# Kernel optimization log

Hardware: AMD Instinct MI355X
Metric: run time of the kernel (lower is better)

Reference implementation:

```python
import jax, jax.numpy as jnp
import numpy as np

NITER = 20
TOL = 1e-10


def setup_inputs() -> dict:
    key = jax.random.key(0)
    n = 8192
    kA, kR, kX = jax.random.split(key, 3)
    # SPD, well-conditioned system matrix: M = A A^T / n + I
    A = jax.random.normal(kA, (n, n), dtype=jnp.float32) * np.float32(1.0 / np.sqrt(n))
    M = A @ A.T + jnp.eye(n, dtype=jnp.float32)
    RHS = jax.random.normal(kR, (n,), dtype=jnp.float32)
    X = jax.random.normal(kX, (n,), dtype=jnp.float32)  # only its shape is used (zeros_like)
    return {"X": X, "M": M, "RHS": RHS}


def reference(X, M, RHS):
    # Faithful port of the TF while_loop CG: max NITER iterations,
    # early-stop condition rTr > 1e-10 emulated by freezing the state
    # (where-select) once converged, keeping fixed shapes under jit.
    X0 = jnp.zeros_like(X)
    r0 = RHS - M @ X0
    p0 = r0
    rTr0 = jnp.sum(r0 * r0)

    def body(carry, _):
        rTr, Xc, r, p = carry
        Ap = M @ p                      # [n] matvec, dominant cost
        rtr = jnp.sum(r * r)            # recomputed in loop body, as in TF source
        alpha = rtr / jnp.sum(p * Ap)
        Xn = Xc + alpha * p
        rn = r - alpha * Ap
        beta = jnp.sum(rn * rn) / rtr
        pn = rn + beta * p
        rTrn = jnp.sum(rn * rn)
        active = rTr > TOL              # while_loop cond on rTr from previous iter
        sel = lambda new, old: jnp.where(active, new, old)
        return (sel(rTrn, rTr), sel(Xn, Xc), sel(rn, r), sel(pn, p)), None

    (_, Xf, _, _), _ = jax.lax.scan(body, (rTr0, X0, r0, p0), None, length=NITER)
    return Xf
```

## Files before the change

### kernel.cpp

```cpp
#include <hip/hip_runtime.h>

#define N 8192
#define NITER 20
#define TOLF 1e-10f

typedef float floatx4 __attribute__((ext_vector_type(4)));
typedef unsigned int uintx4 __attribute__((ext_vector_type(4)));

__device__ __forceinline__ unsigned short f2bf_rne(float f) {
  unsigned int u = __float_as_uint(f);
  unsigned int r = u + 0x7fffu + ((u >> 16) & 1u);
  return (unsigned short)(r >> 16);
}
__device__ __forceinline__ unsigned int pk_bf2(float lo, float hi) {
  return (unsigned int)f2bf_rne(lo) | ((unsigned int)f2bf_rne(hi) << 16);
}
__device__ __forceinline__ float bflo(unsigned int u) { return __uint_as_float(u << 16); }
__device__ __forceinline__ float bfhi(unsigned int u) { return __uint_as_float(u & 0xffff0000u); }

__global__ __launch_bounds__(256) void init_kernel(
    const float* __restrict__ RHS, float* __restrict__ x, float* __restrict__ r,
    float* __restrict__ p, float* __restrict__ rt0) {
  int i = blockIdx.x * 256 + threadIdx.x;
  float v = RHS[i];
  x[i] = 0.0f;
  r[i] = v;
  p[i] = v;
  float val = v * v;
  for (int off = 32; off > 0; off >>= 1) val += __shfl_down(val, off, 64);
  __shared__ float bs[4];
  int wave = threadIdx.x >> 6, lane = threadIdx.x & 63;
  if (lane == 0) bs[wave] = val;
  __syncthreads();
  if (threadIdx.x == 0) atomicAdd(rt0, bs[0] + bs[1] + bs[2] + bs[3]);
}

__device__ __forceinline__ void finish_iteration(
    float* __restrict__ p, float* __restrict__ x, float* __restrict__ r,
    float* __restrict__ Ap, const float* __restrict__ rt,
    float* __restrict__ pap, float* __restrict__ rt_next,
    int* __restrict__ counter, float acc0, float acc1, int row0) {
  int wave = threadIdx.x >> 6, lane = threadIdx.x & 63;
  for (int off = 32; off > 0; off >>= 1) {
    acc0 += __shfl_down(acc0, off, 64);
    acc1 += __shfl_down(acc1, off, 64);
  }
  __shared__ float bs[16];
  __shared__ int tick;
  if (lane == 0) {
    Ap[row0]     = acc0;
    Ap[row0 + 1] = acc1;
    bs[wave] = p[row0] * acc0 + p[row0 + 1] * acc1;
  }
  __syncthreads();
  if (threadIdx.x == 0) {
    float S = 0.0f;
#pragma unroll
    for (int w = 0; w < 16; ++w) S += bs[w];
    __hip_atomic_fetch_add(pap, S, __ATOMIC_RELAXED, __HIP_MEMORY_SCOPE_AGENT);
    tick = __hip_atomic_fetch_add(counter, 1, __ATOMIC_ACQ_REL, __HIP_MEMORY_SCOPE_AGENT);
  }
  __syncthreads();
  if (tick != (int)gridDim.x - 1) return;

  float rtv = *rt;
  bool act = rtv > TOLF;
  if (!act) {
    if (threadIdx.x == 0) *rt_next = rtv;
    return;
  }
  float papv = __hip_atomic_load(pap, __ATOMIC_RELAXED, __HIP_MEMORY_SCOPE_AGENT);
  float alpha = rtv / papv;
  float val = 0.0f;
#pragma unroll
  for (int j = threadIdx.x * 4; j < N; j += 4096) {
    floatx4 pv = *(const floatx4*)(p + j);
    floatx4 av = *(const floatx4*)(Ap + j);
    floatx4 xv = *(const floatx4*)(x + j);
    floatx4 rv = *(const floatx4*)(r + j);
    xv += alpha * pv;
    rv -= alpha * av;
    *(floatx4*)(x + j) = xv;
    *(floatx4*)(r + j) = rv;
    val += rv.x * rv.x + rv.y * rv.y + rv.z * rv.z + rv.w * rv.w;
  }
  for (int off = 32; off > 0; off >>= 1) val += __shfl_down(val, off, 64);
  __shared__ float rs[17];
  if (lane == 0) rs[wave] = val;
  __syncthreads();
  if (threadIdx.x == 0) {
    float S = 0.0f;
#pragma unroll
    for (int w = 0; w < 16; ++w) S += rs[w];
    rs[16] = S;
    *rt_next = S;
  }
  __syncthreads();
  float beta = rs[16] / rtv;
#pragma unroll
  for (int j = threadIdx.x * 4; j < N; j += 4096) {
    floatx4 rv = *(const floatx4*)(r + j);
    floatx4 pv = *(const floatx4*)(p + j);
    pv = rv + beta * pv;
    *(floatx4*)(p + j) = pv;
  }
}

__global__ __launch_bounds__(1024, 4) void cg_iter0_cast(
    const float* __restrict__ M, unsigned short* __restrict__ Mb,
    const float* __restrict__ RHS, float* __restrict__ p, float* __restrict__ Ap,
    float* __restrict__ x, float* __restrict__ r, const float* __restrict__ rt,
    float* __restrict__ pap, float* __restrict__ rt_next, int* __restrict__ counter) {
  int wave = threadIdx.x >> 6, lane = threadIdx.x & 63;
  int row0 = blockIdx.x * 32 + wave * 2;
  const float* M0 = M + (size_t)row0 * N;
  const float* M1 = M0 + N;
  unsigned short* B0 = Mb + (size_t)row0 * N;
  unsigned short* B1 = B0 + N;
  float acc0 = 0.0f, acc1 = 0.0f;
#pragma unroll 2
  for (int c = lane * 8; c < N; c += 512) {
    floatx4 a0 = *(const floatx4*)(M0 + c);
    floatx4 a1 = *(const floatx4*)(M0 + c + 4);
    floatx4 b0 = *(const floatx4*)(M1 + c);
    floatx4 b1 = *(const floatx4*)(M1 + c + 4);
    floatx4 pa = *(const floatx4*)(RHS + c);
    floatx4 pb = *(const floatx4*)(RHS + c + 4);
    acc0 += a0.x * pa.x + a0.y * pa.y + a0.z * pa.z + a0.w * pa.w
          + a1.x * pb.x + a1.y * pb.y + a1.z * pb.z + a1.w * pb.w;
    acc1 += b0.x * pa.x + b0.y * pa.y + b0.z * pa.z + b0.w * pa.w
          + b1.x * pb.x + b1.y * pb.y + b1.z * pb.z + b1.w * pb.w;
    uintx4 o0 = {pk_bf2(a0.x, a0.y), pk_bf2(a0.z, a0.w),
                 pk_bf2(a1.x, a1.y), pk_bf2(a1.z, a1.w)};
    uintx4 o1 = {pk_bf2(b0.x, b0.y), pk_bf2(b0.z, b0.w),
                 pk_bf2(b1.x, b1.y), pk_bf2(b1.z, b1.w)};
    *(uintx4*)(B0 + c) = o0;
    *(uintx4*)(B1 + c) = o1;
  }
  finish_iteration(p, x, r, Ap, rt, pap, rt_next, counter, acc0, acc1, row0);
}

__global__ __launch_bounds__(1024, 4) void cg_iter(
    const unsigned short* __restrict__ Mb, float* __restrict__ p,
    float* __restrict__ Ap, float* __restrict__ x, float* __restrict__ r,
    const float* __restrict__ rt, float* __restrict__ pap,
    float* __restrict__ rt_next, int* __restrict__ counter) {
  int wave = threadIdx.x >> 6, lane = threadIdx.x & 63;
  int row0 = blockIdx.x * 32 + wave * 2;
  const unsigned short* M0 = Mb + (size_t)row0 * N;
  const unsigned short* M1 = M0 + N;
  float acc0 = 0.0f, acc1 = 0.0f;
#pragma unroll 4
  for (int c = lane * 8; c < N; c += 512) {
    uintx4 m0 = *(const uintx4*)(M0 + c);
    uintx4 m1 = *(const uintx4*)(M1 + c);
    floatx4 pa = *(const floatx4*)(p + c);
    floatx4 pb = *(const floatx4*)(p + c + 4);
    acc0 += bflo(m0.x) * pa.x + bfhi(m0.x) * pa.y
          + bflo(m0.y) * pa.z + bfhi(m0.y) * pa.w
          + bflo(m0.z) * pb.x + bfhi(m0.z) * pb.y
          + bflo(m0.w) * pb.z + bfhi(m0.w) * pb.w;
    acc1 += bflo(m1.x) * pa.x + bfhi(m1.x) * pa.y
          + bflo(m1.y) * pa.z + bfhi(m1.y) * pa.w
          + bflo(m1.z) * pb.x + bfhi(m1.z) * pb.y
          + bflo(m1.w) * pb.z + bfhi(m1.w) * pb.w;
  }
  finish_iteration(p, x, r, Ap, rt, pap, rt_next, counter, acc0, acc1, row0);
}

extern "C" void kernel_launch(void* const* d_in, const int* in_sizes, int n_in,
                              void* d_out, int out_size, void* d_ws, size_t ws_size,
                              hipStream_t stream) {
  const float* M   = (const float*)d_in[1];
  const float* RHS = (const float*)d_in[2];
  float* x = (float*)d_out;

  char* ws = (char*)d_ws;
  unsigned short* Mb = (unsigned short*)ws;
  float* Ap = (float*)(ws + (size_t)N * N * 2);
  float* r  = Ap + N;
  float* p  = r + N;
  float* sc = p + N;
  float* RT  = sc;
  float* PAP = sc + 21;
  int*   CNT = (int*)(sc + 41);

  (void)hipMemsetAsync(sc, 0, 61 * sizeof(float), stream);

  init_kernel<<<N / 256, 256, 0, stream>>>(RHS, x, r, p, &RT[0]);
  cg_iter0_cast<<<N / 32, 1024, 0, stream>>>(M, Mb, RHS, p, Ap, x, r,
                                             &RT[0], &PAP[0], &RT[1], &CNT[0]);
  for (int k = 1; k < NITER; ++k) {
    cg_iter<<<N / 32, 1024, 0, stream>>>(Mb, p, Ap, x, r,
                                         &RT[k], &PAP[k], &RT[k + 1], &CNT[k]);
  }
}
```

Measured before the change: 1.015 ms.

## Fuse CG iterations into one persistent cooperative kernel with grid barriers

Result: slower. 2.313 ms (+127.8%).

```diff
diff --git a/kernel.cpp b/kernel.cpp
--- a/kernel.cpp
+++ b/kernel.cpp
@@ -3,6 +3,7 @@
 #define N 8192
 #define NITER 20
 #define TOLF 1e-10f
+#define NBLK 256
 
 typedef float floatx4 __attribute__((ext_vector_type(4)));
 typedef unsigned int uintx4 __attribute__((ext_vector_type(4)));
@@ -18,154 +19,157 @@
 __device__ __forceinline__ float bflo(unsigned int u) { return __uint_as_float(u << 16); }
 __device__ __forceinline__ float bfhi(unsigned int u) { return __uint_as_float(u & 0xffff0000u); }
 
-__global__ __launch_bounds__(256) void init_kernel(
-    const float* __restrict__ RHS, float* __restrict__ x, float* __restrict__ r,
-    float* __restrict__ p, float* __restrict__ rt0) {
-  int i = blockIdx.x * 256 + threadIdx.x;
-  float v = RHS[i];
-  x[i] = 0.0f;
-  r[i] = v;
-  p[i] = v;
-  float val = v * v;
-  for (int off = 32; off > 0; off >>= 1) val += __shfl_down(val, off, 64);
-  __shared__ float bs[4];
-  int wave = threadIdx.x >> 6, lane = threadIdx.x & 63;
-  if (lane == 0) bs[wave] = val;
+__device__ __forceinline__ void grid_sync(int* cnt, int* gen) {
   __syncthreads();
-  if (threadIdx.x == 0) atomicAdd(rt0, bs[0] + bs[1] + bs[2] + bs[3]);
+  if (threadIdx.x == 0) {
+    int g = __hip_atomic_load(gen, __ATOMIC_RELAXED, __HIP_MEMORY_SCOPE_AGENT);
+    int t = __hip_atomic_fetch_add(cnt, 1, __ATOMIC_ACQ_REL, __HIP_MEMORY_SCOPE_AGENT);
+    if (t == NBLK - 1) {
+      __hip_atomic_store(cnt, 0, __ATOMIC_RELAXED, __HIP_MEMORY_SCOPE_AGENT);
+      __hip_atomic_fetch_add(gen, 1, __ATOMIC_ACQ_REL, __HIP_MEMORY_SCOPE_AGENT);
+    } else {
+      while (__hip_atomic_load(gen, __ATOMIC_ACQUIRE, __HIP_MEMORY_SCOPE_AGENT) == g)
+        __builtin_amdgcn_s_sleep(1);
+    }
+  }
+  __syncthreads();
 }
 
-__device__ __forceinline__ void finish_iteration(
-    float* __restrict__ p, float* __restrict__ x, float* __restrict__ r,
-    float* __restrict__ Ap, const float* __restrict__ rt,
-    float* __restrict__ pap, float* __restrict__ rt_next,
-    int* __restrict__ counter, float acc0, float acc1, int row0) {
+__device__ __forceinline__ float sum_part(const float* __restrict__ part, float* lred) {
+  float v = (threadIdx.x < NBLK) ? part[threadIdx.x] : 0.0f;
+  for (int off = 32; off > 0; off >>= 1) v += __shfl_down(v, off, 64);
   int wave = threadIdx.x >> 6, lane = threadIdx.x & 63;
-  for (int off = 32; off > 0; off >>= 1) {
-    acc0 += __shfl_down(acc0, off, 64);
-    acc1 += __shfl_down(acc1, off, 64);
-  }
-  __shared__ float bs[16];
-  __shared__ int tick;
-  if (lane == 0) {
-    Ap[row0]     = acc0;
-    Ap[row0 + 1] = acc1;
-    bs[wave] = p[row0] * acc0 + p[row0 + 1] * acc1;
-  }
+  if (lane == 0) lred[wave] = v;
   __syncthreads();
-  if (threadIdx.x == 0) {
-    float S = 0.0f;
-#pragma unroll
-    for (int w = 0; w < 16; ++w) S += bs[w];
-    __hip_atomic_fetch_add(pap, S, __ATOMIC_RELAXED, __HIP_MEMORY_SCOPE_AGENT);
-    tick = __hip_atomic_fetch_add(counter, 1, __ATOMIC_ACQ_REL, __HIP_MEMORY_SCOPE_AGENT);
-  }
+  float S = lred[0] + lred[1] + lred[2] + lred[3];
   __syncthreads();
-  if (tick != (int)gridDim.x - 1) return;
-
-  float rtv = *rt;
-  bool act = rtv > TOLF;
-  if (!act) {
-    if (threadIdx.x == 0) *rt_next = rtv;
-    return;
-  }
-  float papv = __hip_atomic_load(pap, __ATOMIC_RELAXED, __HIP_MEMORY_SCOPE_AGENT);
-  float alpha = rtv / papv;
-  float val = 0.0f;
-#pragma unroll
-  for (int j = threadIdx.x * 4; j < N; j += 4096) {
-    floatx4 pv = *(const floatx4*)(p + j);
-    floatx4 av = *(const floatx4*)(Ap + j);
-    floatx4 xv = *(const floatx4*)(x + j);
-    floatx4 rv = *(const floatx4*)(r + j);
-    xv += alpha * pv;
-    rv -= alpha * av;
-    *(floatx4*)(x + j) = xv;
-    *(floatx4*)(r + j) = rv;
-    val += rv.x * rv.x + rv.y * rv.y + rv.z * rv.z + rv.w * rv.w;
-  }
-  for (int off = 32; off > 0; off >>= 1) val += __shfl_down(val, off, 64);
-  __shared__ float rs[17];
-  if (lane == 0) rs[wave] = val;
-  __syncthreads();
-  if (threadIdx.x == 0) {
-    float S = 0.0f;
-#pragma unroll
-    for (int w = 0; w < 16; ++w) S += rs[w];
-    rs[16] = S;
-    *rt_next = S;
-  }
-  __syncthreads();
-  float beta = rs[16] / rtv;
-#pragma unroll
-  for (int j = threadIdx.x * 4; j < N; j += 4096) {
-    floatx4 rv = *(const floatx4*)(r + j);
-    floatx4 pv = *(const floatx4*)(p + j);
-    pv = rv + beta * pv;
-    *(floatx4*)(p + j) = pv;
-  }
+  return S;
 }
 
-__global__ __launch_bounds__(1024, 4) void cg_iter0_cast(
+__global__ __launch_bounds__(1024, 4) void cg_persistent(
     const float* __restrict__ M, unsigned short* __restrict__ Mb,
-    const float* __restrict__ RHS, float* __restrict__ p, float* __restrict__ Ap,
-    float* __restrict__ x, float* __restrict__ r, const float* __restrict__ rt,
-    float* __restrict__ pap, float* __restrict__ rt_next, int* __restrict__ counter) {
-  int wave = threadIdx.x >> 6, lane = threadIdx.x & 63;
-  int row0 = blockIdx.x * 32 + wave * 2;
-  const float* M0 = M + (size_t)row0 * N;
-  const float* M1 = M0 + N;
-  unsigned short* B0 = Mb + (size_t)row0 * N;
-  unsigned short* B1 = B0 + N;
-  float acc0 = 0.0f, acc1 = 0.0f;
+    const float* __restrict__ RHS, float* __restrict__ x,
+    float* __restrict__ Ap, float* __restrict__ r, float* __restrict__ p,
+    float* __restrict__ partA, float* __restrict__ partB,
+    int* __restrict__ cnt, int* __restrict__ gen) {
+  int b = blockIdx.x;
+  int t = threadIdx.x;
+  int wave = t >> 6, lane = t & 63;
+  __shared__ float lred[16];
+  __shared__ float bs[16];
+
+  {
+    float val = 0.0f;
+    if (t < 32) {
+      int i = b * 32 + t;
+      float v = RHS[i];
+      x[i] = 0.0f;
+      r[i] = v;
+      p[i] = v;
+      val = v * v;
+    }
+    for (int off = 32; off > 0; off >>= 1) val += __shfl_down(val, off, 64);
+    if (t == 0) partB[b] = val;
+  }
+  grid_sync(cnt, gen);
+  float rt = sum_part(partB, lred);
+
+  int row0 = b * 32 + wave * 2;
+
+  for (int k = 0; k < NITER; ++k) {
+    bool act = rt > TOLF;
+
+    if (act) {
+      float acc0 = 0.0f, acc1 = 0.0f;
+      if (k == 0) {
+        const float* M0 = M + (size_t)row0 * N;
+        const float* M1 = M0 + N;
+        unsigned short* B0 = Mb + (size_t)row0 * N;
+        unsigned short* B1 = B0 + N;
 #pragma unroll 2
-  for (int c = lane * 8; c < N; c += 512) {
-    floatx4 a0 = *(const floatx4*)(M0 + c);
-    floatx4 a1 = *(const floatx4*)(M0 + c + 4);
-    floatx4 b0 = *(const floatx4*)(M1 + c);
-    floatx4 b1 = *(const floatx4*)(M1 + c + 4);
-    floatx4 pa = *(const floatx4*)(RHS + c);
-    floatx4 pb = *(const floatx4*)(RHS + c + 4);
-    acc0 += a0.x * pa.x + a0.y * pa.y + a0.z * pa.z + a0.w * pa.w
-          + a1.x * pb.x + a1.y * pb.y + a1.z * pb.z + a1.w * pb.w;
-    acc1 += b0.x * pa.x + b0.y * pa.y + b0.z * pa.z + b0.w * pa.w
-          + b1.x * pb.x + b1.y * pb.y + b1.z * pb.z + b1.w * pb.w;
-    uintx4 o0 = {pk_bf2(a0.x, a0.y), pk_bf2(a0.z, a0.w),
-                 pk_bf2(a1.x, a1.y), pk_bf2(a1.z, a1.w)};
-    uintx4 o1 = {pk_bf2(b0.x, b0.y), pk_bf2(b0.z, b0.w),
-                 pk_bf2(b1.x, b1.y), pk_bf2(b1.z, b1.w)};
-    *(uintx4*)(B0 + c) = o0;
-    *(uintx4*)(B1 + c) = o1;
+        for (int c = lane * 8; c < N; c += 512) {
+          floatx4 a0 = *(const floatx4*)(M0 + c);
+          floatx4 a1 = *(const floatx4*)(M0 + c + 4);
+          floatx4 b0 = *(const floatx4*)(M1 + c);
+          floatx4 b1 = *(const floatx4*)(M1 + c + 4);
+          floatx4 pa = *(const floatx4*)(p + c);
+          floatx4 pb = *(const floatx4*)(p + c + 4);
+          acc0 += a0.x * pa.x + a0.y * pa.y + a0.z * pa.z + a0.w * pa.w
+                + a1.x * pb.x + a1.y * pb.y + a1.z * pb.z + a1.w * pb.w;
+          acc1 += b0.x * pa.x + b0.y * pa.y + b0.z * pa.z + b0.w * pa.w
+                + b1.x * pb.x + b1.y * pb.y + b1.z * pb.z + b1.w * pb.w;
+          uintx4 o0 = {pk_bf2(a0.x, a0.y), pk_bf2(a0.z, a0.w),
+                       pk_bf2(a1.x, a1.y), pk_bf2(a1.z, a1.w)};
+          uintx4 o1 = {pk_bf2(b0.x, b0.y), pk_bf2(b0.z, b0.w),
+                       pk_bf2(b1.x, b1.y), pk_bf2(b1.z, b1.w)};
+          *(uintx4*)(B0 + c) = o0;
+          *(uintx4*)(B1 + c) = o1;
+        }
+      } else {
+        const unsigned short* M0 = Mb + (size_t)row0 * N;
+        const unsigned short* M1 = M0 + N;
+#pragma unroll 4
+        for (int c = lane * 8; c < N; c += 512) {
+          uintx4 m0 = *(const uintx4*)(M0 + c);
+          uintx4 m1 = *(const uintx4*)(M1 + c);
+          floatx4 pa = *(const floatx4*)(p + c);
+          floatx4 pb = *(const floatx4*)(p + c + 4);
+          acc0 += bflo(m0.x) * pa.x + bfhi(m0.x) * pa.y
+                + bflo(m0.y) * pa.z + bfhi(m0.y) * pa.w
+                + bflo(m0.z) * pb.x + bfhi(m0.z) * pb.y
+                + bflo(m0.w) * pb.z + bfhi(m0.w) * pb.w;
+          acc1 += bflo(m1.x) * pa.x + bfhi(m1.x) * pa.y
+                + bflo(m1.y) * pa.z + bfhi(m1.y) * pa.w
+                + bflo(m1.z) * pb.x + bfhi(m1.z) * pb.y
+                + bflo(m1.w) * pb.z + bfhi(m1.w) * pb.w;
+        }
+      }
+      for (int off = 32; off > 0; off >>= 1) {
+        acc0 += __shfl_down(acc0, off, 64);
+        acc1 += __shfl_down(acc1, off, 64);
+      }
+      if (lane == 0) {
+        Ap[row0] = acc0;
+        Ap[row0 + 1] = acc1;
+        bs[wave] = p[row0] * acc0 + p[row0 + 1] * acc1;
+      }
+      __syncthreads();
+      if (t == 0) {
+        float S = 0.0f;
+#pragma unroll
+        for (int w = 0; w < 16; ++w) S += bs[w];
+        partA[b] = S;
+      }
+    }
+    grid_sync(cnt, gen);
+
+    if (act) {
+      float pap = sum_part(partA, lred);
+      float alpha = rt / pap;
+      float val = 0.0f;
+      if (t < 32) {
+        int i = b * 32 + t;
+        float rv = r[i] - alpha * Ap[i];
+        x[i] += alpha * p[i];
+        r[i] = rv;
+        val = rv * rv;
+      }
+      for (int off = 32; off > 0; off >>= 1) val += __shfl_down(val, off, 64);
+      if (t == 0) partB[b] = val;
+    }
+    grid_sync(cnt, gen);
+
+    if (act) {
+      float rnv = sum_part(partB, lred);
+      float beta = rnv / rt;
+      if (t < 32) {
+        int i = b * 32 + t;
+        p[i] = r[i] + beta * p[i];
+      }
+      rt = rnv;
+    }
+    grid_sync(cnt, gen);
   }
-  finish_iteration(p, x, r, Ap, rt, pap, rt_next, counter, acc0, acc1, row0);
-}
-
-__global__ __launch_bounds__(1024, 4) void cg_iter(
-    const unsigned short* __restrict__ Mb, float* __restrict__ p,
-    float* __restrict__ Ap, float* __restrict__ x, float* __restrict__ r,
-    const float* __restrict__ rt, float* __restrict__ pap,
-    float* __restrict__ rt_next, int* __restrict__ counter) {
-  int wave = threadIdx.x >> 6, lane = threadIdx.x & 63;
-  int row0 = blockIdx.x * 32 + wave * 2;
-  const unsigned short* M0 = Mb + (size_t)row0 * N;
-  const unsigned short* M1 = M0 + N;
-  float acc0 = 0.0f, acc1 = 0.0f;
-#pragma unroll 4
-  for (int c = lane * 8; c < N; c += 512) {
-    uintx4 m0 = *(const uintx4*)(M0 + c);
-    uintx4 m1 = *(const uintx4*)(M1 + c);
-    floatx4 pa = *(const floatx4*)(p + c);
-    floatx4 pb = *(const floatx4*)(p + c + 4);
-    acc0 += bflo(m0.x) * pa.x + bfhi(m0.x) * pa.y
-          + bflo(m0.y) * pa.z + bfhi(m0.y) * pa.w
-          + bflo(m0.z) * pb.x + bfhi(m0.z) * pb.y
-          + bflo(m0.w) * pb.z + bfhi(m0.w) * pb.w;
-    acc1 += bflo(m1.x) * pa.x + bfhi(m1.x) * pa.y
-          + bflo(m1.y) * pa.z + bfhi(m1.y) * pa.w
-          + bflo(m1.z) * pb.x + bfhi(m1.z) * pb.y
-          + bflo(m1.w) * pb.z + bfhi(m1.w) * pb.w;
-  }
-  finish_iteration(p, x, r, Ap, rt, pap, rt_next, counter, acc0, acc1, row0);
 }
 
 extern "C" void kernel_launch(void* const* d_in, const int* in_sizes, int n_in,
@@ -180,18 +184,16 @@
   float* Ap = (float*)(ws + (size_t)N * N * 2);
   float* r  = Ap + N;
   float* p  = r + N;
-  float* sc = p + N;
-  float* RT  = sc;
-  float* PAP = sc + 21;
-  int*   CNT = (int*)(sc + 41);
+  float* partA = p + N;
+  float* partB = partA + NBLK;
+  int* cnt = (int*)(partB + NBLK);
+  int* gen = cnt + 1;
 
-  (void)hipMemsetAsync(sc, 0, 61 * sizeof(float), stream);
+  (void)hipMemsetAsync(cnt, 0, 2 * sizeof(int), stream);
 
-  init_kernel<<<N / 256, 256, 0, stream>>>(RHS, x, r, p, &RT[0]);
-  cg_iter0_cast<<<N / 32, 1024, 0, stream>>>(M, Mb, RHS, p, Ap, x, r,
-                                             &RT[0], &PAP[0], &RT[1], &CNT[0]);
-  for (int k = 1; k < NITER; ++k) {
-    cg_iter<<<N / 32, 1024, 0, stream>>>(Mb, p, Ap, x, r,
-                                         &RT[k], &PAP[k], &RT[k + 1], &CNT[k]);
-  }
+  void* args[] = {(void*)&M, (void*)&Mb, (void*)&RHS, (void*)&x, (void*)&Ap,
+                  (void*)&r, (void*)&p, (void*)&partA, (void*)&partB,
+                  (void*)&cnt, (void*)&gen};
+  (void)hipLaunchCooperativeKernel((void*)cg_persistent, dim3(NBLK), dim3(1024),
+                                   args, 0, stream);
 }
```
